# Optimization experiments

Hardware: AMD Instinct MI355X
Metric: run time of the kernel (lower is better)

## Reference

```python
import jax, jax.numpy as jnp
import numpy as np

B, S, D, H, FF, R = 4, 1024, 1024, 16, 4096, 128
DH = D // H


def rmsnorm(x, w, eps=1e-6):
    # matches torch: norm = ||x||_2 / sqrt(d); out = w * x / (norm + eps)
    n = jnp.sqrt(jnp.sum(x * x, axis=-1, keepdims=True)) / np.sqrt(x.shape[-1]).astype(np.float32)
    return w * x / (n + eps)


def setup_inputs() -> dict:
    key = jax.random.key(0)
    ks = jax.random.split(key, 20)
    def w(k, shape, s=0.02):
        return (jax.random.normal(k, shape, jnp.float32) * s)
    return {
        "x": jax.random.normal(ks[0], (B, S, D), jnp.float32),
        "norm1_w": jnp.ones((D,), jnp.float32),
        "Wq": w(ks[1], (D, D)), "bq": jnp.zeros((D,), jnp.float32),
        "Wk": w(ks[2], (D, D)), "bk": jnp.zeros((D,), jnp.float32),
        "Wv": w(ks[3], (D, D)), "bv": jnp.zeros((D,), jnp.float32),
        "Wz": w(ks[4], (D, D)), "bz": jnp.zeros((D,), jnp.float32),
        "Wg": w(ks[5], (D, D)), "bg": jnp.zeros((D,), jnp.float32),
        "gdw": w(ks[6], (R, D)), "gdb": jnp.zeros((R,), jnp.float32),
        "guw": w(ks[7], (D, R)), "gub": jnp.zeros((D,), jnp.float32),
        "Wo": w(ks[8], (D, D)), "bo": jnp.zeros((D,), jnp.float32),
        "norm2_w": jnp.ones((D,), jnp.float32),
        "f1w": w(ks[9], (FF, D)), "f1b": jnp.zeros((FF,), jnp.float32),
        "f2w": w(ks[10], (D, FF)), "f2b": jnp.zeros((D,), jnp.float32),
    }


def reference(x, norm1_w, Wq, bq, Wk, bk, Wv, bv, Wz, bz, Wg, bg,
              gdw, gdb, guw, gub, Wo, bo, norm2_w, f1w, f1b, f2w, f2b):
    b, s, d = x.shape
    h = d // DH
    # 1. Norm + Q/K/V/Z projections
    xn = rmsnorm(x, norm1_w)
    q = xn @ Wq.T + bq
    k = xn @ Wk.T + bk
    v = xn @ Wv.T + bv
    z = xn @ Wz.T + bz
    # 2-3. DPG decay: gamma_t = clamp(sigmoid(W_up ReLU(W_down z_t)))
    gamma = jax.nn.sigmoid(jax.nn.relu(z @ gdw.T + gdb) @ guw.T + gub)
    gamma = jnp.clip(gamma, 1e-6, 1.0 - 1e-6)
    # 4. Core recurrence: h_t = z_t * sigmoid(W_g h_{t-1}) + gamma_t * h_{t-1}
    def step(hprev, zg):
        zt, gt = zg
        hn = zt * jax.nn.sigmoid(hprev @ Wg.T + bg) + gt * hprev
        return hn, hn
    h0 = jnp.zeros((b, d), x.dtype)
    _, hs = jax.lax.scan(step, h0, (jnp.swapaxes(z, 0, 1), jnp.swapaxes(gamma, 0, 1)))
    hseq = jnp.swapaxes(hs, 0, 1)  # [B,S,D]
    # 5. Multi-head attention over Q,K,V
    qh = q.reshape(b, s, h, DH)
    kh = k.reshape(b, s, h, DH)
    vh = v.reshape(b, s, h, DH)
    scores = jnp.einsum('bqhd,bkhd->bhqk', qh, kh) / np.sqrt(DH).astype(np.float32)
    attn = jax.nn.softmax(scores, axis=-1)
    ao = jnp.einsum('bhqk,bkhd->bqhd', attn, vh).reshape(b, s, d)
    ao = ao @ Wo.T + bo
    # 6. Residuals
    y = x + ao + hseq
    # 7. FFN + output
    yn = rmsnorm(y, norm2_w)
    ff = jax.nn.gelu(yn @ f1w.T + f1b) @ f2w.T + f2b
    return y + ff
```

## Files before the change

kernel.cpp:

```cpp
#include <hip/hip_runtime.h>
#include <stdint.h>

#define DD 1024
#define SS 1024
#define NBS 32

typedef __attribute__((ext_vector_type(8))) __bf16 bf16x8;
typedef __attribute__((ext_vector_type(4))) float f32x4;

union Frag { uint4 u; bf16x8 b; };

__device__ __forceinline__ float bf2f(ushort u){ union{uint32_t i; float f;} c; c.i = ((uint32_t)u)<<16; return c.f; }
__device__ __forceinline__ float bflo(uint32_t p){ union{uint32_t i; float f;} c; c.i = p<<16; return c.f; }
__device__ __forceinline__ float bfhi(uint32_t p){ union{uint32_t i; float f;} c; c.i = p & 0xffff0000u; return c.f; }
__device__ __forceinline__ ushort f2bf(float f){
  union{float f; uint32_t u;} c; c.f = f;
  uint32_t u = c.u;
  return (ushort)((u + 0x7fffu + ((u>>16)&1u)) >> 16);
}

__global__ __launch_bounds__(256) void cast_k(const float* __restrict__ s,
    ushort* __restrict__ d, int n)
{
  int i = (blockIdx.x*256 + threadIdx.x)*4;
  if (i >= n) return;
  float4 v = *(const float4*)(s+i);
  ushort4 o; o.x=f2bf(v.x); o.y=f2bf(v.y); o.z=f2bf(v.z); o.w=f2bf(v.w);
  *(ushort4*)(d+i) = o;
}

__global__ __launch_bounds__(256) void rmsnorm_k(const float* __restrict__ X,
    const float* __restrict__ w, ushort* __restrict__ out)
{
  const int row = blockIdx.x, t = threadIdx.x;
  const float* x = X + (size_t)row*DD;
  float xs[4]; float s = 0.f;
  #pragma unroll
  for (int i=0;i<4;i++){ float v = x[t + i*256]; xs[i]=v; s += v*v; }
  #pragma unroll
  for (int off=32; off>0; off>>=1) s += __shfl_xor(s, off, 64);
  __shared__ float sred[4];
  if ((t&63)==0) sred[t>>6] = s;
  __syncthreads();
  s = sred[0]+sred[1]+sred[2]+sred[3];
  float inv = 1.f/(sqrtf(s)*0.03125f + 1e-6f);
  #pragma unroll
  for (int i=0;i<4;i++){
    int c2 = t + i*256;
    out[(size_t)row*DD + c2] = f2bf(xs[i]*inv*w[c2]);
  }
}

enum { ACT_NONE=0, ACT_RELU=1, ACT_SIG=2, ACT_GELU=3 };
enum { EPI_B16=0, EPI_DUAL=1, EPI_F32=2, EPI_Y=3, EPI_OUT=4 };

template<int ACT, int EPI>
__global__ __launch_bounds__(256) void gemm_bt(
    const ushort* __restrict__ A, const ushort* __restrict__ W,
    const float* __restrict__ bias, int N, int K,
    ushort* __restrict__ Ob, float* __restrict__ Of,
    const float* __restrict__ X32, const ushort* __restrict__ H16,
    const float* __restrict__ Yf)
{
  __shared__ __align__(16) ushort At[128*32];
  __shared__ __align__(16) ushort Wt[128*32];
  const int tid = threadIdx.x;
  const int wave = tid >> 6, lane = tid & 63;
  const int quad = lane >> 4, l16 = lane & 15;
  const int wr = wave >> 1, wc = wave & 1;
  const int m0 = blockIdx.x * 128, n0 = blockIdx.y * 128;

  f32x4 acc[4][4];
  const f32x4 vz = {0.f,0.f,0.f,0.f};
  #pragma unroll
  for (int i=0;i<4;i++)
    #pragma unroll
    for (int j=0;j<4;j++) acc[i][j] = vz;

  const ushort* gA = A + (size_t)(m0 + wave*32 + (lane>>2))*K + (lane&3)*8;
  const ushort* gW = W + (size_t)(n0 + wave*32 + (lane>>2))*K + (lane&3)*8;
  ushort* lA = At + wave*1024 + lane*8;
  ushort* lW = Wt + wave*1024 + lane*8;

  for (int ko = 0; ko < K; ko += 32) {
    uint4 va  = *(const uint4*)(gA + ko);
    uint4 va2 = *(const uint4*)(gA + ko + (size_t)16*K);
    uint4 vw  = *(const uint4*)(gW + ko);
    uint4 vw2 = *(const uint4*)(gW + ko + (size_t)16*K);
    __syncthreads();
    *(uint4*)lA          = va;
    *(uint4*)(lA + 512)  = va2;
    *(uint4*)lW          = vw;
    *(uint4*)(lW + 512)  = vw2;
    __syncthreads();
    Frag af[4], bfr[4];
    #pragma unroll
    for (int mi=0;mi<4;mi++)
      af[mi].u = *(const uint4*)&At[(wr*64 + mi*16 + l16)*32 + quad*8];
    #pragma unroll
    for (int ni=0;ni<4;ni++)
      bfr[ni].u = *(const uint4*)&Wt[(wc*64 + ni*16 + l16)*32 + quad*8];
    #pragma unroll
    for (int mi=0;mi<4;mi++)
      #pragma unroll
      for (int ni=0;ni<4;ni++)
        acc[mi][ni] = __builtin_amdgcn_mfma_f32_16x16x32_bf16(af[mi].b, bfr[ni].b, acc[mi][ni], 0,0,0);
  }

  float bia[4];
  #pragma unroll
  for (int ni=0;ni<4;ni++) bia[ni] = bias[n0 + wc*64 + ni*16 + l16];
  #pragma unroll
  for (int mi=0;mi<4;mi++) {
    const int row0 = m0 + wr*64 + mi*16 + quad*4;
    #pragma unroll
    for (int ni=0;ni<4;ni++) {
      const int col = n0 + wc*64 + ni*16 + l16;
      #pragma unroll
      for (int r=0;r<4;r++) {
        float vx = acc[mi][ni][r] + bia[ni];
        if (ACT == ACT_RELU) vx = fmaxf(vx, 0.f);
        else if (ACT == ACT_SIG) {
          vx = 1.f/(1.f+__expf(-vx));
          vx = fminf(fmaxf(vx, 1e-6f), 1.f-1e-6f);
        } else if (ACT == ACT_GELU) {
          float ci = 0.7978845608028654f*(vx + 0.044715f*vx*vx*vx);
          float th = 1.f - 2.f/(1.f + __expf(2.f*ci));
          vx = 0.5f*vx*(1.f+th);
        }
        size_t idx = (size_t)(row0 + r)*N + col;
        if (EPI == EPI_B16)      Ob[idx] = f2bf(vx);
        else if (EPI == EPI_DUAL){ Ob[idx] = f2bf(vx); Of[idx] = vx; }
        else if (EPI == EPI_F32)  Of[idx] = vx;
        else if (EPI == EPI_Y)    Of[idx] = vx + X32[idx] + bf2f(H16[idx]);
        else                      Of[idx] = vx + Yf[idx];
      }
    }
  }
}

__global__ __launch_bounds__(256) void attn_k(const ushort* __restrict__ q,
  const ushort* __restrict__ k, const ushort* __restrict__ v, ushort* __restrict__ ao)
{
  __shared__ __align__(16) ushort Ks[64*64];
  __shared__ __align__(16) ushort Vs[64*64];
  __shared__ float Ps[64*65];
  const int qt = blockIdx.x, bh = blockIdx.y;
  const int b = bh >> 4, h = bh & 15;
  const int t = threadIdx.x, r = t >> 2, seg = t & 3;
  const ushort* qrow = q + ((size_t)(b*SS + qt*64 + r))*DD + h*64;
  float qr[64];
  #pragma unroll
  for (int i=0;i<64;i+=8){
    uint4 u = *(const uint4*)(qrow + i);
    qr[i+0]=bflo(u.x); qr[i+1]=bfhi(u.x); qr[i+2]=bflo(u.y); qr[i+3]=bfhi(u.y);
    qr[i+4]=bflo(u.z); qr[i+5]=bfhi(u.z); qr[i+6]=bflo(u.w); qr[i+7]=bfhi(u.w);
  }
  float o[16];
  #pragma unroll
  for (int i=0;i<16;i++) o[i]=0.f;
  float mrun = -1e30f, lrun = 0.f;
  const int jrow = t >> 3, jch = t & 7;
  for (int kt=0; kt<16; kt++) {
    __syncthreads();
    const ushort* kg = k + ((size_t)(b*SS + kt*64))*DD + h*64;
    const ushort* vg = v + ((size_t)(b*SS + kt*64))*DD + h*64;
    #pragma unroll
    for (int part=0; part<2; part++){
      int j = jrow + part*32;
      *(uint4*)&Ks[j*64 + jch*8] = *(const uint4*)(kg + (size_t)j*DD + jch*8);
      *(uint4*)&Vs[j*64 + jch*8] = *(const uint4*)(vg + (size_t)j*DD + jch*8);
    }
    __syncthreads();
    float sc[16];
    #pragma unroll
    for (int jj=0;jj<16;jj++){
      int j = seg*16 + jj;
      float s_ = 0.f;
      #pragma unroll
      for (int i=0;i<64;i+=8){
        uint4 u = *(const uint4*)&Ks[j*64+i];
        s_ = fmaf(qr[i+0], bflo(u.x), s_); s_ = fmaf(qr[i+1], bfhi(u.x), s_);
        s_ = fmaf(qr[i+2], bflo(u.y), s_); s_ = fmaf(qr[i+3], bfhi(u.y), s_);
        s_ = fmaf(qr[i+4], bflo(u.z), s_); s_ = fmaf(qr[i+5], bfhi(u.z), s_);
        s_ = fmaf(qr[i+6], bflo(u.w), s_); s_ = fmaf(qr[i+7], bfhi(u.w), s_);
      }
      sc[jj] = s_ * 0.125f;
    }
    float mx = sc[0];
    #pragma unroll
    for (int jj=1;jj<16;jj++) mx = fmaxf(mx, sc[jj]);
    mx = fmaxf(mx, __shfl_xor(mx, 1, 64));
    mx = fmaxf(mx, __shfl_xor(mx, 2, 64));
    float mnew = fmaxf(mrun, mx);
    float psum = 0.f;
    #pragma unroll
    for (int jj=0;jj<16;jj++){
      float p = __expf(sc[jj]-mnew);
      Ps[r*65 + seg*16 + jj] = p;
      psum += p;
    }
    psum += __shfl_xor(psum, 1, 64);
    psum += __shfl_xor(psum, 2, 64);
    float alpha = __expf(mrun - mnew);
    lrun = lrun*alpha + psum;
    mrun = mnew;
    #pragma unroll
    for (int i=0;i<16;i++) o[i] *= alpha;
    __syncthreads();
    #pragma unroll 4
    for (int j=0;j<64;j++){
      float pj = Ps[r*65 + j];
      uint4 u0 = *(const uint4*)&Vs[j*64 + seg*16];
      uint4 u1 = *(const uint4*)&Vs[j*64 + seg*16 + 8];
      o[ 0]=fmaf(pj,bflo(u0.x),o[ 0]); o[ 1]=fmaf(pj,bfhi(u0.x),o[ 1]);
      o[ 2]=fmaf(pj,bflo(u0.y),o[ 2]); o[ 3]=fmaf(pj,bfhi(u0.y),o[ 3]);
      o[ 4]=fmaf(pj,bflo(u0.z),o[ 4]); o[ 5]=fmaf(pj,bfhi(u0.z),o[ 5]);
      o[ 6]=fmaf(pj,bflo(u0.w),o[ 6]); o[ 7]=fmaf(pj,bfhi(u0.w),o[ 7]);
      o[ 8]=fmaf(pj,bflo(u1.x),o[ 8]); o[ 9]=fmaf(pj,bfhi(u1.x),o[ 9]);
      o[10]=fmaf(pj,bflo(u1.y),o[10]); o[11]=fmaf(pj,bfhi(u1.y),o[11]);
      o[12]=fmaf(pj,bflo(u1.z),o[12]); o[13]=fmaf(pj,bfhi(u1.z),o[13]);
      o[14]=fmaf(pj,bflo(u1.w),o[14]); o[15]=fmaf(pj,bfhi(u1.w),o[15]);
    }
  }
  float invl = 1.f/lrun;
  ushort* orow = ao + ((size_t)(b*SS + qt*64 + r))*DD + h*64 + seg*16;
  #pragma unroll
  for (int i=0;i<16;i++) orow[i] = f2bf(o[i]*invl);
}

__global__ __launch_bounds__(256) void scan_k(
    const ushort* __restrict__ Wgb, const float* __restrict__ bg,
    const float* __restrict__ z32, const float* __restrict__ gm32,
    ushort* __restrict__ hseq, ushort* __restrict__ hstate)
{
  const int blk = blockIdx.x, t = threadIdx.x;
  const int wave = t>>6, lane = t&63, quad = lane>>4, c = lane&15;
  const int mt = wave & 1, kh = wave >> 1;
  const int nbase = blk*32 + mt*16;
  const bool epi = (kh == 0) && (c < 4);
  const int n0w = nbase + quad*4;
  Frag a[16];
  {
    const ushort* wrow = Wgb + (size_t)(nbase + c)*DD + kh*512 + quad*8;
    #pragma unroll
    for (int kt=0;kt<16;kt++) a[kt].u = *(const uint4*)(wrow + kt*32);
  }
  float bgv[4];
  #pragma unroll
  for (int r=0;r<4;r++) bgv[r] = bg[nbase + quad*4 + r];
  __shared__ __align__(16) ushort Hs[4096];
  __shared__ float redbuf[2][64][5];
  const int di = (c*1024 + n0w) >> 1;
  int gmax = 256;

  for (int st=0; st<SS; st++) {
    float zr[4], gr[4];
    if (epi) {
      float4 z4 = *(const float4*)(z32  + ((size_t)c*SS + st)*DD + n0w);
      float4 g4 = *(const float4*)(gm32 + ((size_t)c*SS + st)*DD + n0w);
      zr[0]=z4.x; zr[1]=z4.y; zr[2]=z4.z; zr[3]=z4.w;
      gr[0]=g4.x; gr[1]=g4.y; gr[2]=g4.z; gr[3]=g4.w;
    }
    if (st > 0) {
      const uint32_t* hrd = (const uint32_t*)(hstate + ((st+3)&3)*4096);
      uint32_t vals[8];
      int guard = 0;
      for (;;) {
        bool ok = true;
        #pragma unroll
        for (int i=0;i<8;i++)
          vals[i] = __hip_atomic_load(hrd + t + i*256, __ATOMIC_RELAXED, __HIP_MEMORY_SCOPE_AGENT);
        #pragma unroll
        for (int i=0;i<8;i++) ok &= (vals[i] != 0xFFFFFFFFu);
        if (ok) break;
        if (++guard > gmax) { gmax = 0; break; }
        __builtin_amdgcn_s_sleep(2);
      }
      if (epi) {
        uint32_t* rst = (uint32_t*)(hstate + ((st+2)&3)*4096);
        __hip_atomic_store(rst + di,     0xFFFFFFFFu, __ATOMIC_RELAXED, __HIP_MEMORY_SCOPE_AGENT);
        __hip_atomic_store(rst + di + 1, 0xFFFFFFFFu, __ATOMIC_RELAXED, __HIP_MEMORY_SCOPE_AGENT);
      }
      uint32_t* hsd = (uint32_t*)Hs;
      #pragma unroll
      for (int i=0;i<8;i++) hsd[t + i*256] = vals[i];
      __syncthreads();
    }
    f32x4 acc = {0.f,0.f,0.f,0.f};
    if (st > 0) {
      f32x4 acc1 = {0.f,0.f,0.f,0.f};
      const uint4 z4 = make_uint4(0u,0u,0u,0u);
      #pragma unroll
      for (int kt=0;kt<16;kt+=2) {
        Frag b0, b1;
        b0.u = (c<4) ? *(const uint4*)&Hs[c*1024 + kh*512 + (kt  )*32 + quad*8] : z4;
        b1.u = (c<4) ? *(const uint4*)&Hs[c*1024 + kh*512 + (kt+1)*32 + quad*8] : z4;
        acc  = __builtin_amdgcn_mfma_f32_16x16x32_bf16(a[kt  ].b, b0.b, acc,  0,0,0);
        acc1 = __builtin_amdgcn_mfma_f32_16x16x32_bf16(a[kt+1].b, b1.b, acc1, 0,0,0);
      }
      #pragma unroll
      for (int r=0;r<4;r++) acc[r] += acc1[r];
    }
    if (kh == 1) {
      #pragma unroll
      for (int r=0;r<4;r++) redbuf[mt][lane][r] = acc[r];
    }
    __syncthreads();
    if (epi) {
      ushort hb[4];
      #pragma unroll
      for (int r=0;r<4;r++) {
        float g = acc[r] + redbuf[mt][lane][r] + bgv[r];
        g = 1.f/(1.f+__expf(-g));
        float hp = (st>0) ? bf2f(Hs[c*1024 + n0w + r]) : 0.f;
        hb[r] = f2bf(zr[r]*g + gr[r]*hp);
      }
      uint32_t p0 = (uint32_t)hb[0] | ((uint32_t)hb[1]<<16);
      uint32_t p1 = (uint32_t)hb[2] | ((uint32_t)hb[3]<<16);
      uint32_t* hwd = (uint32_t*)(hstate + (st&3)*4096);
      __hip_atomic_store(hwd + di,     p0, __ATOMIC_RELAXED, __HIP_MEMORY_SCOPE_AGENT);
      __hip_atomic_store(hwd + di + 1, p1, __ATOMIC_RELAXED, __HIP_MEMORY_SCOPE_AGENT);
      uint32_t* sq = (uint32_t*)(hseq + ((size_t)c*SS + st)*DD + n0w);
      sq[0] = p0; sq[1] = p1;
    }
    __syncthreads();
  }
}

extern "C" void kernel_launch(void* const* d_in, const int* in_sizes, int n_in,
                              void* d_out, int out_size, void* d_ws, size_t ws_size,
                              hipStream_t stream)
{
  const float* x   = (const float*)d_in[0];
  const float* n1w = (const float*)d_in[1];
  const float* Wq  = (const float*)d_in[2];
  const float* bq  = (const float*)d_in[3];
  const float* Wk  = (const float*)d_in[4];
  const float* bk  = (const float*)d_in[5];
  const float* Wv  = (const float*)d_in[6];
  const float* bv  = (const float*)d_in[7];
  const float* Wz  = (const float*)d_in[8];
  const float* bz  = (const float*)d_in[9];
  const float* Wg_ = (const float*)d_in[10];
  const float* bg  = (const float*)d_in[11];
  const float* gdw = (const float*)d_in[12];
  const float* gdb = (const float*)d_in[13];
  const float* guw = (const float*)d_in[14];
  const float* gub = (const float*)d_in[15];
  const float* Wo  = (const float*)d_in[16];
  const float* bo  = (const float*)d_in[17];
  const float* n2w = (const float*)d_in[18];
  const float* f1w = (const float*)d_in[19];
  const float* f1b = (const float*)d_in[20];
  const float* f2w = (const float*)d_in[21];
  const float* f2b = (const float*)d_in[22];

  char* ws = (char*)d_ws;
  const size_t MB = (size_t)1<<20;
  ushort* Wqb  = (ushort*)(ws +  0*MB);
  ushort* Wkb  = (ushort*)(ws +  2*MB);
  ushort* Wvb  = (ushort*)(ws +  4*MB);
  ushort* Wzb  = (ushort*)(ws +  6*MB);
  ushort* Wob  = (ushort*)(ws +  8*MB);
  ushort* Wgb  = (ushort*)(ws + 10*MB);
  ushort* gdwb = (ushort*)(ws + 12*MB);
  ushort* guwb = (ushort*)(ws + 12*MB + (512<<10));
  ushort* f1wb = (ushort*)(ws + 13*MB);
  ushort* f2wb = (ushort*)(ws + 21*MB);
  ushort* xn   = (ushort*)(ws + 29*MB);
  ushort* qb   = (ushort*)(ws + 37*MB);
  ushort* kb   = (ushort*)(ws + 45*MB);
  ushort* vb   = (ushort*)(ws + 53*MB);
  ushort* zb16 = (ushort*)(ws + 61*MB);
  ushort* ff1  = (ushort*)(ws + 37*MB);
  ushort* t1   = (ushort*)(ws + 69*MB);
  ushort* hseq = (ushort*)(ws + 70*MB);
  ushort* aob  = (ushort*)(ws + 78*MB);
  float*  zb32 = (float*) (ws + 86*MB);
  float*  yf   = (float*) (ws + 86*MB);
  float*  gm32 = (float*) (ws +102*MB);
  ushort* hst  = (ushort*)(ws +118*MB);
  ushort* yn = xn;

  cast_k<<<1024, 256, 0, stream>>>(Wq,  Wqb, 1048576);
  cast_k<<<1024, 256, 0, stream>>>(Wk,  Wkb, 1048576);
  cast_k<<<1024, 256, 0, stream>>>(Wv,  Wvb, 1048576);
  cast_k<<<1024, 256, 0, stream>>>(Wz,  Wzb, 1048576);
  cast_k<<<1024, 256, 0, stream>>>(Wo,  Wob, 1048576);
  cast_k<<<1024, 256, 0, stream>>>(Wg_, Wgb, 1048576);
  cast_k<<< 128, 256, 0, stream>>>(gdw, gdwb, 131072);
  cast_k<<< 128, 256, 0, stream>>>(guw, guwb, 131072);
  cast_k<<<4096, 256, 0, stream>>>(f1w, f1wb, 4194304);
  cast_k<<<4096, 256, 0, stream>>>(f2w, f2wb, 4194304);
  rmsnorm_k<<<4096, 256, 0, stream>>>(x, n1w, xn);
  gemm_bt<ACT_NONE,EPI_B16 ><<<dim3(32,8), 256, 0, stream>>>(xn, Wqb, bq, 1024, 1024, qb,  nullptr, nullptr, nullptr, nullptr);
  gemm_bt<ACT_NONE,EPI_B16 ><<<dim3(32,8), 256, 0, stream>>>(xn, Wkb, bk, 1024, 1024, kb,  nullptr, nullptr, nullptr, nullptr);
  gemm_bt<ACT_NONE,EPI_B16 ><<<dim3(32,8), 256, 0, stream>>>(xn, Wvb, bv, 1024, 1024, vb,  nullptr, nullptr, nullptr, nullptr);
  gemm_bt<ACT_NONE,EPI_DUAL><<<dim3(32,8), 256, 0, stream>>>(xn, Wzb, bz, 1024, 1024, zb16, zb32,   nullptr, nullptr, nullptr);
  gemm_bt<ACT_RELU,EPI_B16><<<dim3(32,1), 256, 0, stream>>>(zb16, gdwb, gdb, 128, 1024, t1, nullptr, nullptr, nullptr, nullptr);
  gemm_bt<ACT_SIG ,EPI_F32><<<dim3(32,8), 256, 0, stream>>>(t1, guwb, gub, 1024, 128, nullptr, gm32, nullptr, nullptr, nullptr);
  attn_k<<<dim3(16,64), 256, 0, stream>>>(qb, kb, vb, aob);
  (void)hipMemsetAsync(hst, 0xFF, 32768, stream);
  scan_k<<<dim3(NBS), 256, 0, stream>>>(Wgb, bg, zb32, gm32, hseq, hst);
  gemm_bt<ACT_NONE,EPI_Y><<<dim3(32,8), 256, 0, stream>>>(aob, Wob, bo, 1024, 1024, nullptr, yf, x, hseq, nullptr);
  rmsnorm_k<<<4096, 256, 0, stream>>>(yf, n2w, yn);
  gemm_bt<ACT_GELU,EPI_B16><<<dim3(32,32), 256, 0, stream>>>(yn, f1wb, f1b, 4096, 1024, ff1, nullptr, nullptr, nullptr, nullptr);
  gemm_bt<ACT_NONE,EPI_OUT><<<dim3(32,8), 256, 0, stream>>>(ff1, f2wb, f2b, 1024, 4096, nullptr, (float*)d_out, nullptr, nullptr, yf);
}
```

Baseline: 4.949 ms.

## Tighten recurrence step: 64-bit atomics, prefetch z/gamma, lighter barriers

Each step of the serial recurrence kernel now polls and publishes the shared hidden state with 64-bit atomics instead of 32-bit ones. The next step's z and gamma values are prefetched into registers, and the poll sleep interval is shortened. __syncthreads is replaced by an inline lgkmcnt wait plus s_barrier, so the global prefetch loads no longer have to drain at each barrier. The aim is to shorten the per-step latency of the 1024-step serial chain, at the risk of memory-ordering subtleties when the barriers no longer wait on vmcnt.

Result: no change. 4.927 ms (-0.4%).

```diff
diff --git a/kernel.cpp b/kernel.cpp
--- a/kernel.cpp
+++ b/kernel.cpp
@@ -251,41 +251,48 @@
   for (int r=0;r<4;r++) bgv[r] = bg[nbase + quad*4 + r];
   __shared__ __align__(16) ushort Hs[4096];
   __shared__ float redbuf[2][64][5];
-  const int di = (c*1024 + n0w) >> 1;
+  const int qi = (c*1024 + n0w) >> 2;
   int gmax = 256;
 
+  float4 znx = {0,0,0,0}, gnx = {0,0,0,0};
+  if (epi) {
+    znx = *(const float4*)(z32  + ((size_t)c*SS + 0)*DD + n0w);
+    gnx = *(const float4*)(gm32 + ((size_t)c*SS + 0)*DD + n0w);
+  }
+
   for (int st=0; st<SS; st++) {
-    float zr[4], gr[4];
-    if (epi) {
-      float4 z4 = *(const float4*)(z32  + ((size_t)c*SS + st)*DD + n0w);
-      float4 g4 = *(const float4*)(gm32 + ((size_t)c*SS + st)*DD + n0w);
-      zr[0]=z4.x; zr[1]=z4.y; zr[2]=z4.z; zr[3]=z4.w;
-      gr[0]=g4.x; gr[1]=g4.y; gr[2]=g4.z; gr[3]=g4.w;
-    }
     if (st > 0) {
-      const uint32_t* hrd = (const uint32_t*)(hstate + ((st+3)&3)*4096);
-      uint32_t vals[8];
+      const uint64_t* hrd = (const uint64_t*)(hstate + ((st+3)&3)*4096);
+      uint64_t v0,v1,v2,v3;
       int guard = 0;
       for (;;) {
-        bool ok = true;
-        #pragma unroll
-        for (int i=0;i<8;i++)
-          vals[i] = __hip_atomic_load(hrd + t + i*256, __ATOMIC_RELAXED, __HIP_MEMORY_SCOPE_AGENT);
-        #pragma unroll
-        for (int i=0;i<8;i++) ok &= (vals[i] != 0xFFFFFFFFu);
+        v0 = __hip_atomic_load(hrd + t*4 + 0, __ATOMIC_RELAXED, __HIP_MEMORY_SCOPE_AGENT);
+        v1 = __hip_atomic_load(hrd + t*4 + 1, __ATOMIC_RELAXED, __HIP_MEMORY_SCOPE_AGENT);
+        v2 = __hip_atomic_load(hrd + t*4 + 2, __ATOMIC_RELAXED, __HIP_MEMORY_SCOPE_AGENT);
+        v3 = __hip_atomic_load(hrd + t*4 + 3, __ATOMIC_RELAXED, __HIP_MEMORY_SCOPE_AGENT);
+        bool ok = ((uint32_t)v0 != 0xFFFFFFFFu) & ((uint32_t)(v0>>32) != 0xFFFFFFFFu)
+                & ((uint32_t)v1 != 0xFFFFFFFFu) & ((uint32_t)(v1>>32) != 0xFFFFFFFFu)
+                & ((uint32_t)v2 != 0xFFFFFFFFu) & ((uint32_t)(v2>>32) != 0xFFFFFFFFu)
+                & ((uint32_t)v3 != 0xFFFFFFFFu) & ((uint32_t)(v3>>32) != 0xFFFFFFFFu);
         if (ok) break;
         if (++guard > gmax) { gmax = 0; break; }
-        __builtin_amdgcn_s_sleep(2);
+        __builtin_amdgcn_s_sleep(1);
       }
       if (epi) {
-        uint32_t* rst = (uint32_t*)(hstate + ((st+2)&3)*4096);
-        __hip_atomic_store(rst + di,     0xFFFFFFFFu, __ATOMIC_RELAXED, __HIP_MEMORY_SCOPE_AGENT);
-        __hip_atomic_store(rst + di + 1, 0xFFFFFFFFu, __ATOMIC_RELAXED, __HIP_MEMORY_SCOPE_AGENT);
-      }
-      uint32_t* hsd = (uint32_t*)Hs;
-      #pragma unroll
-      for (int i=0;i<8;i++) hsd[t + i*256] = vals[i];
-      __syncthreads();
+        uint64_t* rst = (uint64_t*)(hstate + ((st+2)&3)*4096);
+        __hip_atomic_store(rst + qi, 0xFFFFFFFFFFFFFFFFull,
+                           __ATOMIC_RELAXED, __HIP_MEMORY_SCOPE_AGENT);
+      }
+      uint64_t* hsd = (uint64_t*)Hs;
+      hsd[t*4+0]=v0; hsd[t*4+1]=v1; hsd[t*4+2]=v2; hsd[t*4+3]=v3;
+    }
+    float4 zc = znx, gc = gnx;
+    if (epi && (st+1 < SS)) {
+      znx = *(const float4*)(z32  + ((size_t)c*SS + (st+1))*DD + n0w);
+      gnx = *(const float4*)(gm32 + ((size_t)c*SS + (st+1))*DD + n0w);
+    }
+    if (st > 0) {
+      asm volatile("s_waitcnt lgkmcnt(0)\ns_barrier" ::: "memory");
     }
     f32x4 acc = {0.f,0.f,0.f,0.f};
     if (st > 0) {
@@ -306,9 +313,11 @@
       #pragma unroll
       for (int r=0;r<4;r++) redbuf[mt][lane][r] = acc[r];
     }
-    __syncthreads();
+    asm volatile("s_waitcnt lgkmcnt(0)\ns_barrier" ::: "memory");
     if (epi) {
       ushort hb[4];
+      float zr[4] = {zc.x, zc.y, zc.z, zc.w};
+      float gr[4] = {gc.x, gc.y, gc.z, gc.w};
       #pragma unroll
       for (int r=0;r<4;r++) {
         float g = acc[r] + redbuf[mt][lane][r] + bgv[r];
@@ -318,13 +327,13 @@
       }
       uint32_t p0 = (uint32_t)hb[0] | ((uint32_t)hb[1]<<16);
       uint32_t p1 = (uint32_t)hb[2] | ((uint32_t)hb[3]<<16);
-      uint32_t* hwd = (uint32_t*)(hstate + (st&3)*4096);
-      __hip_atomic_store(hwd + di,     p0, __ATOMIC_RELAXED, __HIP_MEMORY_SCOPE_AGENT);
-      __hip_atomic_store(hwd + di + 1, p1, __ATOMIC_RELAXED, __HIP_MEMORY_SCOPE_AGENT);
-      uint32_t* sq = (uint32_t*)(hseq + ((size_t)c*SS + st)*DD + n0w);
-      sq[0] = p0; sq[1] = p1;
-    }
-    __syncthreads();
+      uint64_t pk = ((uint64_t)p1<<32) | (uint64_t)p0;
+      uint64_t* hwd = (uint64_t*)(hstate + (st&3)*4096);
+      __hip_atomic_store(hwd + qi, pk, __ATOMIC_RELAXED, __HIP_MEMORY_SCOPE_AGENT);
+      uint2* sq = (uint2*)(hseq + ((size_t)c*SS + st)*DD + n0w);
+      *sq = make_uint2(p0, p1);
+    }
+    asm volatile("s_waitcnt lgkmcnt(0)\ns_barrier" ::: "memory");
   }
 }
 
```
